# Optimization experiments

Measured on AMD Instinct MI355X. Metric: run time of the kernel, lower is better.

## Reference

```python
import jax, jax.numpy as jnp
import numpy as np

B, T, D = 16, 1024, 256
H, DK = 2, 128          # n_head, d_k = d_v = D // n_head
K = 5                   # conv kernel size
TEMP = float(np.sqrt(D))  # temperature = d_model ** 0.5


def mish(x):
    return x * jnp.tanh(jax.nn.softplus(x))


def setup_inputs() -> dict:
    key = jax.random.key(0)
    ks = jax.random.split(key, 16)
    s = 0.02
    p = lambda k, shp: jax.random.normal(k, shp, dtype=jnp.float32) * s
    inp = {
        'x': jax.random.normal(ks[0], (B, T, D), dtype=jnp.float32),
        'mask': jax.random.randint(ks[1], (B, T), 0, 2).astype(bool),
        # spectral MLP
        'W1': p(ks[2], (D, D)), 'b1': p(ks[3], (D,)),
        'W2': p(ks[4], (D, D)), 'b2': p(ks[5], (D,)),
        # two Conv1dGLU blocks: Conv1d(D -> 2D, k=5), torch layout [out,in,k]
        'cW1': p(ks[6], (2 * D, D, K)), 'cb1': p(ks[7], (2 * D,)),
        'cW2': p(ks[8], (2 * D, D, K)), 'cb2': p(ks[9], (2 * D,)),
        # attention projections (torch Linear: y = x @ W.T + b)
        'Wq': p(ks[10], (D, D)), 'bq': p(ks[11], (D,)),
        'Wk': p(ks[12], (D, D)), 'bk': p(ks[13], (D,)),
        'Wv': p(ks[14], (D, D)), 'bv': p(ks[15], (D,)),
        'Wo': p(jax.random.fold_in(key, 100), (D, D)),
        'bo': p(jax.random.fold_in(key, 101), (D,)),
        # final fc
        'Wf': p(jax.random.fold_in(key, 102), (D, D)),
        'bf': p(jax.random.fold_in(key, 103), (D,)),
    }
    return inp


def conv1d_glu(h, w, b):
    # h: [B, C, T]; w: [2C, C, K]; 'same' padding, GLU gate + residual
    y = jax.lax.conv_general_dilated(h, w, window_strides=(1,), padding=[(K // 2, K // 2)],
                                     dimension_numbers=('NCH', 'OIH', 'NCH'))
    y = y + b[None, :, None]
    a, g = jnp.split(y, 2, axis=1)
    return h + a * jax.nn.sigmoid(g)


def reference(x, mask, W1, b1, W2, b2, cW1, cb1, cW2, cb2,
              Wq, bq, Wk, bk, Wv, bv, Wo, bo, Wf, bf):
    # spectral: Linear + Mish (dropout is identity at inference)
    h = mish(x @ W1.T + b1)
    h = mish(h @ W2.T + b2)
    # temporal: two Conv1dGLU residual blocks over [B, C, T]
    h = h.transpose(0, 2, 1)
    h = conv1d_glu(h, cW1, cb1)
    h = conv1d_glu(h, cW2, cb2)
    h = h.transpose(0, 2, 1)
    # zero out padded frames
    h = jnp.where(mask[:, :, None], 0.0, h)
    residual = h
    # multi-head self-attention; mask hides padded keys
    q = (h @ Wq.T + bq).reshape(B, T, H, DK)
    k = (h @ Wk.T + bk).reshape(B, T, H, DK)
    v = (h @ Wv.T + bv).reshape(B, T, H, DK)
    attn = jnp.einsum('bqhd,bkhd->bhqk', q, k) / TEMP
    attn = jnp.where(mask[:, None, None, :], -jnp.inf, attn)
    attn = jax.nn.softmax(attn, axis=-1)
    out = jnp.einsum('bhqk,bkhd->bqhd', attn, v).reshape(B, T, D)
    h = out @ Wo.T + bo + residual
    # final projection + masked temporal average pool
    y = h @ Wf.T + bf
    len_ = (~mask).sum(axis=1, keepdims=True).astype(y.dtype)  # [B,1]
    y = jnp.where(mask[:, :, None], 0.0, y)
    w = y.sum(axis=1) / len_
    return w
```

## Files before the change

### kernel.cpp

```cpp
#include <hip/hip_runtime.h>
#include <hip/hip_bf16.h>
#include <math.h>


#define DEV __device__ __forceinline__

static constexpr int B_ = 16, T_ = 1024, D_ = 256;
static constexpr int N_ = B_ * T_;

typedef __attribute__((ext_vector_type(8))) short bf16x8;
typedef __attribute__((ext_vector_type(16))) float floatx16;

DEV float sigmoidf_(float x) { return 1.f / (1.f + __expf(-x)); }
DEV float mishf_(float x) {
  float u = __expf(fminf(x, 30.f));
  float t = u * (u + 2.f);
  return x * (t / (t + 2.f));
}
DEV ushort f2bf_(float x) {
  __hip_bfloat16 h = __float2bfloat16(x);
  return *(ushort*)&h;
}

__global__ __launch_bounds__(256) void prep_all_kernel(
    const unsigned* __restrict__ mraw,
    const float* __restrict__ W1, const float* __restrict__ W2,
    const float* __restrict__ Wq, const float* __restrict__ Wk,
    const float* __restrict__ Wv, const float* __restrict__ Wo,
    const float* __restrict__ cW1, const float* __restrict__ cW2,
    ushort* __restrict__ w1, ushort* __restrict__ w2,
    ushort* __restrict__ wqkv, ushort* __restrict__ wo,
    ushort* __restrict__ WtF1, ushort* __restrict__ WtF2,
    float* __restrict__ fmask, ushort* __restrict__ QF,
    ushort* __restrict__ KF, float* __restrict__ pooled) {
  int bid = blockIdx.x, tid = threadIdx.x;
  if (bid < 384) {
    int i = bid * 256 + tid;
    int widx = i >> 14, r = i & 16383;
    const float* src;
    ushort* dst;
    switch (widx) {
      case 0: src = W1; dst = w1; break;
      case 1: src = W2; dst = w2; break;
      case 2: src = Wq; dst = wqkv; break;
      case 3: src = Wk; dst = wqkv + 65536; break;
      case 4: src = Wv; dst = wqkv + 131072; break;
      default: src = Wo; dst = wo; break;
    }
    float4 v = ((const float4*)src)[r];
    ushort4 u;
    u.x = f2bf_(v.x); u.y = f2bf_(v.y); u.z = f2bf_(v.z); u.w = f2bf_(v.w);
    ((ushort4*)dst)[r] = u;
  } else if (bid < 1024) {
    int idx = (bid - 384) * 256 + tid;
    const float* cw = (idx < 81920) ? cW1 : cW2;
    ushort* dst = (idx < 81920) ? WtF1 : WtF2;
    int i8 = (idx < 81920) ? idx : idx - 81920;
    int i = i8 * 8;
    int half = (i >> 3) & 1, m31 = (i >> 4) & 31;
    int frag = i >> 9;
    int ks = frag & 1, c = (frag >> 1) & 7, tap = (frag >> 4) % 5,
        cot = frag / 80;
    int co = cot * 32 + m31;
    int cin0 = c * 32 + ks * 16 + half * 8;
    ushort u[8];
#pragma unroll
    for (int j = 0; j < 8; ++j)
      u[j] = f2bf_(cw[(size_t)(co * 256 + cin0 + j) * 5 + tap]);
    *(uint4*)&dst[i] = *(uint4*)u;
  } else {
    int isByte = 0, isFloat = 0;
    for (int i = 0; i < 16; ++i) {
      unsigned v = mraw[tid * 16 + i];
      if (v == 0x3F800000u) isFloat = 1;
      else if (v > 1u) isByte = 1;
    }
    __shared__ int sByte, sFloat;
    if (tid == 0) { sByte = 0; sFloat = 0; }
    __syncthreads();
    if (isByte) atomicOr(&sByte, 1);
    if (isFloat) atomicOr(&sFloat, 1);
    __syncthreads();
    int mode = sFloat ? 2 : (sByte ? 1 : 0);
    int mb = bid - 1024;
    int id = mb * 256 + tid;
    int bh = id >> 10, t = id & 1023, b = bh >> 1;
    int gidx = b * 1024 + t;
    unsigned mv;
    if (mode == 1) mv = ((const unsigned char*)mraw)[gidx];
    else           mv = mraw[gidx];
    float fm = (mv != 0u) ? 1.f : 0.f;
    if ((bh & 1) == 0) fmask[gidx] = fm;
    if (mb < 16) pooled[mb * 256 + tid] = 0.f;
    size_t qb = ((size_t)(bh * 32 + (t >> 5)) * 9 + 8) * 512 + (t & 31) * 16;
    QF[qb] = f2bf_(1.f);
#pragma unroll
    for (int j = 1; j < 16; ++j) QF[qb + j] = 0;
    size_t kb = ((size_t)(bh * 32 + (t >> 5)) * 9 + 8) * 512 + (t & 31) * 16;
    KF[kb] = (fm != 0.f) ? f2bf_(-60000.f) : (ushort)0;
#pragma unroll
    for (int j = 1; j < 16; ++j) KF[kb + j] = 0;
  }
}

template <int ACT, int RESID, int OMODE, int AF32>
__global__ __launch_bounds__(256, 4) void gemm_mfma_kernel(
    const void* __restrict__ Av, const ushort* __restrict__ W16,
    const float* __restrict__ bias, const float* __restrict__ resid,
    const float* __restrict__ fmask,
    float* __restrict__ outf, ushort* __restrict__ outb) {
  __shared__ __align__(16) ushort As[2][32 * 72];
  int tid = threadIdx.x;
  int w = tid >> 6, lane = tid & 63;
  int m31 = lane & 31, half = lane >> 5;
  int n0 = blockIdx.x * 32;
  int col = blockIdx.y * 128 + w * 32 + m31;
  const ushort* A16 = (const ushort*)Av;
  const float* A32 = (const float*)Av;
  int srow = tid >> 3, spart = tid & 7;

  floatx16 acc;
#pragma unroll
  for (int i = 0; i < 16; ++i) acc[i] = 0.f;

  auto stageA = [&](int buf, int k0) {
    if (AF32) {
      float4 v0 = *(const float4*)&A32[(size_t)(n0 + srow) * 256 + k0 + spart * 8];
      float4 v1 = *(const float4*)&A32[(size_t)(n0 + srow) * 256 + k0 + spart * 8 + 4];
      ushort u[8];
      u[0] = f2bf_(v0.x); u[1] = f2bf_(v0.y); u[2] = f2bf_(v0.z); u[3] = f2bf_(v0.w);
      u[4] = f2bf_(v1.x); u[5] = f2bf_(v1.y); u[6] = f2bf_(v1.z); u[7] = f2bf_(v1.w);
      *(uint4*)&As[buf][srow * 72 + spart * 8] = *(uint4*)u;
    } else {
      *(uint4*)&As[buf][srow * 72 + spart * 8] =
          *(const uint4*)&A16[(size_t)(n0 + srow) * 256 + k0 + spart * 8];
    }
  };
  stageA(0, 0);
  bf16x8 bn[4];
#pragma unroll
  for (int ks = 0; ks < 4; ++ks)
    bn[ks] = *(const bf16x8*)&W16[(size_t)col * 256 + ks * 16 + half * 8];

  for (int c = 0; c < 4; ++c) {
    __syncthreads();
    if (c < 3) stageA((c + 1) & 1, (c + 1) * 64);
    bf16x8 bc[4] = {bn[0], bn[1], bn[2], bn[3]};
    if (c < 3) {
      int k0 = (c + 1) * 64;
#pragma unroll
      for (int ks = 0; ks < 4; ++ks)
        bn[ks] = *(const bf16x8*)&W16[(size_t)col * 256 + k0 + ks * 16 + half * 8];
    }
    const ushort* ab = As[c & 1];
#pragma unroll
    for (int ks = 0; ks < 4; ++ks) {
      bf16x8 af = *(const bf16x8*)&ab[m31 * 72 + ks * 16 + half * 8];
      acc = __builtin_amdgcn_mfma_f32_32x32x16_bf16(af, bc[ks], acc, 0, 0, 0);
    }
  }
  float bv = bias[col];
  if (OMODE == 3) {
    int b = n0 >> 10;
    float psum = 0.f;
#pragma unroll
    for (int reg = 0; reg < 16; ++reg) {
      int row = n0 + (reg & 3) + 8 * (reg >> 2) + 4 * half;
      float keep = (fmask[row] == 0.f) ? 1.f : 0.f;
      psum += keep * (acc[reg] + bv + resid[(size_t)row * 256 + col]);
    }
    atomicAdd(&outf[b * 256 + col], psum);
    return;
  }
#pragma unroll
  for (int reg = 0; reg < 16; ++reg) {
    int row = n0 + (reg & 3) + 8 * (reg >> 2) + 4 * half;
    float v = acc[reg] + bv;
    if (ACT == 1) v = mishf_(v);
    if (RESID) v += resid[(size_t)row * 256 + col];
    if (OMODE == 0) {
      outf[(size_t)row * 256 + col] = v;
    } else if (OMODE == 1) {
      outb[(size_t)row * 256 + col] = f2bf_(v);
    } else {
      outf[(size_t)row * 256 + col] = v;
      outb[(size_t)row * 256 + col] = f2bf_(v);
    }
  }
}

__global__ __launch_bounds__(256, 4) void qkv_mfma_kernel(
    const ushort* __restrict__ A16, const ushort* __restrict__ wqkv,
    const float* __restrict__ bq, const float* __restrict__ bk,
    const float* __restrict__ bv,
    ushort* __restrict__ QF, ushort* __restrict__ KF, ushort* __restrict__ VF) {
  __shared__ __align__(16) ushort As[2][32 * 72];
  __shared__ __align__(16) ushort Tw[4][32 * 40];
  int tid = threadIdx.x;
  int w = tid >> 6, lane = tid & 63;
  int m31 = lane & 31, half = lane >> 5;
  int n0 = blockIdx.x * 32;
  int by = blockIdx.z;
  const ushort* W16 = wqkv + (size_t)by * 65536;
  const float* bias = (by == 0) ? bq : (by == 1) ? bk : bv;
  int col = blockIdx.y * 128 + w * 32 + m31;
  int srow = tid >> 3, spart = tid & 7;

  floatx16 acc;
#pragma unroll
  for (int i = 0; i < 16; ++i) acc[i] = 0.f;

  *(uint4*)&As[0][srow * 72 + spart * 8] =
      *(const uint4*)&A16[(size_t)(n0 + srow) * 256 + spart * 8];
  bf16x8 bn[4];
#pragma unroll
  for (int ks = 0; ks < 4; ++ks)
    bn[ks] = *(const bf16x8*)&W16[(size_t)col * 256 + ks * 16 + half * 8];

  for (int c = 0; c < 4; ++c) {
    __syncthreads();
    if (c < 3) {
      int k0 = (c + 1) * 64;
      *(uint4*)&As[(c + 1) & 1][srow * 72 + spart * 8] =
          *(const uint4*)&A16[(size_t)(n0 + srow) * 256 + k0 + spart * 8];
    }
    bf16x8 bc[4] = {bn[0], bn[1], bn[2], bn[3]};
    if (c < 3) {
      int k0 = (c + 1) * 64;
#pragma unroll
      for (int ks = 0; ks < 4; ++ks)
        bn[ks] = *(const bf16x8*)&W16[(size_t)col * 256 + k0 + ks * 16 + half * 8];
    }
    const ushort* ab = As[c & 1];
#pragma unroll
    for (int ks = 0; ks < 4; ++ks) {
      bf16x8 af = *(const bf16x8*)&ab[m31 * 72 + ks * 16 + half * 8];
      acc = __builtin_amdgcn_mfma_f32_32x32x16_bf16(af, bc[ks], acc, 0, 0, 0);
    }
  }
  int b = n0 >> 10;
  float bvv = bias[col];
  int h = col >> 7, d127 = col & 127;
  int bh = b * 2 + h;
  if (by == 2) {
    int ctv = d127 >> 5, m31v = d127 & 31;
#pragma unroll
    for (int rg = 0; rg < 4; ++rg) {
      int t0 = (n0 & 1023) + 8 * rg + 4 * half;
      ushort4 u;
      u.x = f2bf_(acc[rg * 4 + 0] + bvv);
      u.y = f2bf_(acc[rg * 4 + 1] + bvv);
      u.z = f2bf_(acc[rg * 4 + 2] + bvv);
      u.w = f2bf_(acc[rg * 4 + 3] + bvv);
      size_t addr = ((size_t)(bh * 16 + (t0 >> 6)) * 16 +
                     ((t0 >> 4) & 3) * 4 + ctv) * 512 +
                    m31v * 16 + ((t0 >> 3) & 1) * 8 + (t0 & 7);
      *(ushort4*)&VF[addr] = u;
    }
  } else {
    float scale = (by == 0) ? 0.0625f : 1.f;
    ushort* tw = &Tw[w][0];
#pragma unroll
    for (int reg = 0; reg < 16; ++reg) {
      int brow = (reg & 3) + 8 * (reg >> 2) + 4 * half;
      tw[brow * 40 + m31] = f2bf_((acc[reg] + bvv) * scale);
    }
    ushort* dst = (by == 0) ? QF : KF;
    int tile9 = (bh * 32 + ((n0 & 1023) >> 5)) * 9;
    int c0 = ((blockIdx.y * 128 + w * 32) & 127) >> 4;
    int tr = lane >> 1, hb = lane & 1;
#pragma unroll
    for (int cc = 0; cc < 2; ++cc) {
      uint4 v = *(const uint4*)&tw[tr * 40 + cc * 16 + hb * 8];
      *(uint4*)&dst[(size_t)(tile9 + c0 + cc) * 512 + lane * 8] = v;
    }
  }
}

template <int DO_MASK>
__global__ __launch_bounds__(256, 4) void conv_mfma_kernel(
    const ushort* __restrict__ H16, const float* __restrict__ Hf,
    const ushort* __restrict__ WtF, const float* __restrict__ cb,
    const float* __restrict__ fmask, float* __restrict__ outf,
    ushort* __restrict__ outb) {
  __shared__ __align__(16) ushort As[2][68 * 72];
  int tid = threadIdx.x;
  int w = tid >> 6, lane = tid & 63;
  int m31 = lane & 31, half = lane >> 5;
  int wr = w >> 1, wc = w & 1;
  int n0 = blockIdx.x * 64;
  int cg = blockIdx.y;
  int tbase = n0 & 1023;
  int acol = cg * 64 + wc * 32;
  int cotA = cg * 2 + wc, cotG = 8 + cg * 2 + wc;

  floatx16 acc[2];
#pragma unroll
  for (int ct = 0; ct < 2; ++ct)
#pragma unroll
    for (int i = 0; i < 16; ++i) acc[ct][i] = 0.f;

  auto stageA = [&](int buf, int k0) {
    for (int i = tid; i < 544; i += 256) {
      int row = i >> 3, part = i & 7;
      int t = tbase + row - 2;
      uint4 v = make_uint4(0u, 0u, 0u, 0u);
      if ((unsigned)t < 1024u)
        v = *(const uint4*)&H16[(size_t)(n0 + row - 2) * 256 + k0 + part * 8];
      *(uint4*)&As[buf][row * 72 + part * 8] = v;
    }
  };
  stageA(0, 0);

  for (int c = 0; c < 4; ++c) {
    __syncthreads();
    if (c < 3) stageA((c + 1) & 1, (c + 1) * 64);
    const ushort* ab = As[c & 1];
#pragma unroll
    for (int tap = 0; tap < 5; ++tap) {
      int fA = ((cotA * 5 + tap) * 8 + c * 2) * 2;
      int fG = ((cotG * 5 + tap) * 8 + c * 2) * 2;
      bf16x8 ba[4], bg[4];
#pragma unroll
      for (int q = 0; q < 4; ++q) {
        ba[q] = *(const bf16x8*)&WtF[(size_t)(fA + q) * 512 + m31 * 16 + half * 8];
        bg[q] = *(const bf16x8*)&WtF[(size_t)(fG + q) * 512 + m31 * 16 + half * 8];
      }
#pragma unroll
      for (int ks = 0; ks < 4; ++ks) {
        bf16x8 af = *(const bf16x8*)&ab[(wr * 32 + m31 + tap) * 72 +
                                        ks * 16 + half * 8];
        acc[0] = __builtin_amdgcn_mfma_f32_32x32x16_bf16(af, ba[ks], acc[0], 0, 0, 0);
        acc[1] = __builtin_amdgcn_mfma_f32_32x32x16_bf16(af, bg[ks], acc[1], 0, 0, 0);
      }
    }
  }
  int col = acol + m31;
  float ba = cb[col], bg = cb[256 + col];
#pragma unroll
  for (int reg = 0; reg < 16; ++reg) {
    int brow = wr * 32 + (reg & 3) + 8 * (reg >> 2) + 4 * half;
    int grow = n0 + brow;
    float a = acc[0][reg] + ba;
    float g = acc[1][reg] + bg;
    float v = Hf[(size_t)grow * 256 + col] + a * sigmoidf_(g);
    if (DO_MASK) {
      if (fmask[grow] != 0.f) v = 0.f;
    }
    outf[(size_t)grow * 256 + col] = v;
    outb[(size_t)grow * 256 + col] = f2bf_(v);
  }
}

__global__ __launch_bounds__(256, 2) void attn_mfma4_kernel(
    const ushort* __restrict__ QF, const ushort* __restrict__ KF,
    const ushort* __restrict__ VF, ushort* __restrict__ O) {
  __shared__ __align__(16) ushort Sm[2][17408];
  __shared__ float Ml[2][2][32];
  int tid = threadIdx.x;
  int w = tid >> 6, lane = tid & 63;
  int m31 = lane & 31, half = lane >> 5;
  int qt = w & 1, kh = w >> 1;
  int bh = blockIdx.x;
  int q0 = blockIdx.y * 64 + qt * 32;
  int lpos = m31 * 16 + half * 8;

  bf16x8 qe[9];
  {
    int qtile9 = (bh * 32 + (q0 >> 5)) * 9;
#pragma unroll
    for (int c = 0; c < 9; ++c)
      qe[c] = *(const bf16x8*)&QF[(size_t)(qtile9 + c) * 512 + lpos];
  }
  floatx16 oacc[4];
#pragma unroll
  for (int ct = 0; ct < 4; ++ct)
#pragma unroll
    for (int i = 0; i < 16; ++i) oacc[ct][i] = 0.f;
  float mi = -1e30f, li = 0.f;

  auto stage = [&](int it, int buf) {
    const ushort* k0src = KF + (size_t)(bh * 32 + it) * 4608;
    const ushort* k1src = KF + (size_t)(bh * 32 + 16 + it) * 4608;
    const ushort* v0src =
        VF + (size_t)((bh * 16 + (it >> 1)) * 16 + (it & 1) * 8) * 512;
    const ushort* v1src =
        VF + (size_t)((bh * 16 + 8 + (it >> 1)) * 16 + (it & 1) * 8) * 512;
    auto copyc = [&](int c) {
      const ushort* src;
      int idx;
      if (c < 576)       { src = k0src; idx = c; }
      else if (c < 1152) { src = k1src; idx = c - 576; }
      else if (c < 1664) { src = v0src; idx = c - 1152; }
      else               { src = v1src; idx = c - 1664; }
      uint4 v = *(const uint4*)(src + idx * 8);
      *(uint4*)&Sm[buf][c * 8] = v;
    };
#pragma unroll
    for (int k = 0; k < 8; ++k) copyc(tid + k * 256);
    if (tid < 128) copyc(2048 + tid);
  };

  stage(0, 0);
  for (int it = 0; it < 16; ++it) {
    __syncthreads();
    int buf = it & 1;
    const ushort* Kb = &Sm[buf][kh * 4608];
    const ushort* Vb = &Sm[buf][9216 + kh * 4096];
    floatx16 s0;
#pragma unroll
    for (int i = 0; i < 16; ++i) s0[i] = 0.f;
#pragma unroll
    for (int c = 0; c < 9; ++c) {
      bf16x8 kf = *(const bf16x8*)&Kb[c * 512 + lpos];
      s0 = __builtin_amdgcn_mfma_f32_32x32x16_bf16(kf, qe[c], s0, 0, 0, 0);
    }
    float mloc = s0[0];
#pragma unroll
    for (int r = 1; r < 16; ++r) mloc = fmaxf(mloc, s0[r]);
    float mt = fmaxf(mloc, __shfl_xor(mloc, 32));
    float mnew = fmaxf(mi, mt);
    float alpha = __expf(mi - mnew);
    bool dead = (mnew <= -3.0e4f);
    float sum = 0.f;
#pragma unroll
    for (int r = 0; r < 16; ++r) {
      float v = dead ? 0.f : __expf(s0[r] - mnew);
      s0[r] = v;
      sum += v;
    }
    sum += __shfl_xor(sum, 32);
    li = li * alpha + sum;
    mi = mnew;
#pragma unroll
    for (int ct = 0; ct < 4; ++ct)
#pragma unroll
      for (int i = 0; i < 16; ++i) oacc[ct][i] *= alpha;
    float tx[16];
#pragma unroll
    for (int r = 0; r < 16; ++r) tx[r] = __shfl_xor(s0[r], 32);
    bf16x8 pf[2];
#pragma unroll
    for (int s = 0; s < 2; ++s) {
      union { bf16x8 v; ushort u[8]; } pk;
#pragma unroll
      for (int j = 0; j < 8; ++j) {
        int base = s * 8;
        float own = s0[base + j];
        float lo = (j < 4) ? own : tx[base + j - 4];
        float hi = (j < 4) ? tx[base + 4 + j] : own;
        pk.u[j] = f2bf_(half ? hi : lo);
      }
      pf[s] = pk.v;
    }
#pragma unroll
    for (int s2 = 0; s2 < 2; ++s2)
#pragma unroll
      for (int ct = 0; ct < 4; ++ct) {
        bf16x8 vf = *(const bf16x8*)&Vb[(s2 * 4 + ct) * 512 + lpos];
        oacc[ct] = __builtin_amdgcn_mfma_f32_32x32x16_bf16(
            vf, pf[s2], oacc[ct], 0, 0, 0);
      }
    if (it < 15) stage(it + 1, (it + 1) & 1);
  }
  float* Opf = (float*)&Sm[0][0];
  if (kh == 1) {
#pragma unroll
    for (int ct = 0; ct < 4; ++ct)
#pragma unroll
      for (int r = 0; r < 16; ++r) {
        int dv = ct * 32 + (r & 3) + 8 * (r >> 2) + 4 * half;
        Opf[(qt * 128 + dv) * 33 + m31] = oacc[ct][r];
      }
    if (half == 0) { Ml[qt][0][m31] = mi; Ml[qt][1][m31] = li; }
  }
  __syncthreads();
  if (kh == 0) {
    float mB = Ml[qt][0][m31], lB = Ml[qt][1][m31];
    float m = fmaxf(mi, mB);
    float aA = __expf(mi - m), aB = __expf(mB - m);
    float l = li * aA + lB * aB;
    float inv = (l > 0.f) ? 1.f / l : 0.f;
    int b = bh >> 1, h = bh & 1;
    size_t rowbase = (size_t)(b * 1024 + q0 + m31) * 256 + h * 128;
#pragma unroll
    for (int ct = 0; ct < 4; ++ct)
#pragma unroll
      for (int rg = 0; rg < 4; ++rg) {
        int dv0 = ct * 32 + 8 * rg + 4 * half;
        ushort4 u;
        u.x = f2bf_((oacc[ct][rg * 4 + 0] * aA + Opf[(qt * 128 + dv0 + 0) * 33 + m31] * aB) * inv);
        u.y = f2bf_((oacc[ct][rg * 4 + 1] * aA + Opf[(qt * 128 + dv0 + 1) * 33 + m31] * aB) * inv);
        u.z = f2bf_((oacc[ct][rg * 4 + 2] * aA + Opf[(qt * 128 + dv0 + 2) * 33 + m31] * aB) * inv);
        u.w = f2bf_((oacc[ct][rg * 4 + 3] * aA + Opf[(qt * 128 + dv0 + 3) * 33 + m31] * aB) * inv);
        *(ushort4*)&O[rowbase + dv0] = u;
      }
  }
}

__global__ __launch_bounds__(256) void final_kernel(
    const float* __restrict__ pooled, const float* __restrict__ fmask,
    const float* __restrict__ Wf, const float* __restrict__ bf,
    float* __restrict__ out) {
  int b = blockIdx.x, j = threadIdx.x;
  __shared__ __align__(16) float p[256];
  __shared__ float red[256];
  p[j] = pooled[b * 256 + j];
  float c = 0.f;
  for (int i = 0; i < 4; ++i)
    c += (fmask[b * 1024 + i * 256 + j] == 0.f) ? 1.f : 0.f;
  red[j] = c;
  __syncthreads();
  for (int st = 128; st > 0; st >>= 1) {
    if (j < st) red[j] += red[j + st];
    __syncthreads();
  }
  float len = red[0];
  const float* wrow = Wf + (size_t)j * 256;
  float acc = 0.f;
  for (int d4 = 0; d4 < 64; ++d4) {
    float4 wv = ((const float4*)wrow)[d4];
    float4 pv = ((const float4*)p)[d4];
    acc += wv.x * pv.x + wv.y * pv.y + wv.z * pv.z + wv.w * pv.w;
  }
  float inv = (len > 0.f) ? 1.f / len : 0.f;
  out[b * 256 + j] = acc * inv + bf[j];
}

extern "C" void kernel_launch(void* const* d_in, const int* in_sizes, int n_in,
                              void* d_out, int out_size, void* d_ws, size_t ws_size,
                              hipStream_t stream) {
  const float* x      = (const float*)d_in[0];
  const unsigned* msk = (const unsigned*)d_in[1];
  const float* W1 = (const float*)d_in[2];
  const float* b1 = (const float*)d_in[3];
  const float* W2 = (const float*)d_in[4];
  const float* b2 = (const float*)d_in[5];
  const float* cW1 = (const float*)d_in[6];
  const float* cb1 = (const float*)d_in[7];
  const float* cW2 = (const float*)d_in[8];
  const float* cb2 = (const float*)d_in[9];
  const float* Wq = (const float*)d_in[10];
  const float* bq = (const float*)d_in[11];
  const float* Wk = (const float*)d_in[12];
  const float* bk = (const float*)d_in[13];
  const float* Wv = (const float*)d_in[14];
  const float* bv = (const float*)d_in[15];
  const float* Wo = (const float*)d_in[16];
  const float* bo = (const float*)d_in[17];
  const float* Wf = (const float*)d_in[18];
  const float* bf = (const float*)d_in[19];
  float* out = (float*)d_out;

  float* ws = (float*)d_ws;
  size_t ND = (size_t)N_ * D_;
  float* F0      = ws;
  float* F1      = F0 + ND;
  float* fmask   = F1 + ND;
  float* pooled  = fmask + N_;
  ushort* G0 = (ushort*)(pooled + 16 * 256);
  ushort* G1 = G0 + ND;
  ushort* QF = G1 + ND;
  ushort* KF = QF + (size_t)32 * 32 * 9 * 512;
  ushort* VF = KF + (size_t)32 * 32 * 9 * 512;
  ushort* w1_16 = VF + (size_t)32 * 16 * 16 * 512;
  ushort* w2_16 = w1_16 + 65536;
  ushort* wo_16 = w2_16 + 65536;
  ushort* wqkv  = wo_16 + 65536;
  ushort* WtF1  = wqkv + 3 * 65536;
  ushort* WtF2  = WtF1 + 655360;

  dim3 blk(256);
  prep_all_kernel<<<dim3(1152), blk, 0, stream>>>(
      msk, W1, W2, Wq, Wk, Wv, Wo, cW1, cW2,
      w1_16, w2_16, wqkv, wo_16, WtF1, WtF2, fmask, QF, KF, pooled);
  gemm_mfma_kernel<1, 0, 1, 1><<<dim3(512, 2), blk, 0, stream>>>(
      x, w1_16, b1, nullptr, nullptr, nullptr, G1);
  gemm_mfma_kernel<1, 0, 2, 0><<<dim3(512, 2), blk, 0, stream>>>(
      G1, w2_16, b2, nullptr, nullptr, F0, G0);
  conv_mfma_kernel<0><<<dim3(256, 4), blk, 0, stream>>>(
      G0, F0, WtF1, cb1, fmask, F1, G1);
  conv_mfma_kernel<1><<<dim3(256, 4), blk, 0, stream>>>(
      G1, F1, WtF2, cb2, fmask, F0, G0);
  qkv_mfma_kernel<<<dim3(512, 2, 3), blk, 0, stream>>>(
      G0, wqkv, bq, bk, bv, QF, KF, VF);
  attn_mfma4_kernel<<<dim3(32, 16), blk, 0, stream>>>(QF, KF, VF, G1);
  gemm_mfma_kernel<0, 1, 3, 0><<<dim3(512, 2), blk, 0, stream>>>(
      G1, wo_16, bo, F0, fmask, pooled, nullptr);
  final_kernel<<<dim3(16), blk, 0, stream>>>(pooled, fmask, Wf, bf, out);
}
```

Baseline: 282.6 us.

## Split global-to-LDS staging into register prefetch and deferred LDS write

In the GEMM, QKV projection, conv-GLU and attention kernels, the next tile's global loads are now issued into registers at the top of each iteration. They are written to shared memory only after the MFMA work on the current tile finishes. The aim is to hide global-load latency behind compute instead of stalling on each load before its LDS store. This raises register pressure, which can lower occupancy, notably the 9 uint4 staging registers in the attention kernel.

```diff
diff --git a/kernel.cpp b/kernel.cpp
--- a/kernel.cpp
+++ b/kernel.cpp
@@ -123,20 +123,28 @@
 #pragma unroll
   for (int i = 0; i < 16; ++i) acc[i] = 0.f;
 
-  auto stageA = [&](int buf, int k0) {
+  uint4 areg;
+  float4 af0, af1;
+  auto loadA = [&](int k0) {
     if (AF32) {
-      float4 v0 = *(const float4*)&A32[(size_t)(n0 + srow) * 256 + k0 + spart * 8];
-      float4 v1 = *(const float4*)&A32[(size_t)(n0 + srow) * 256 + k0 + spart * 8 + 4];
+      af0 = *(const float4*)&A32[(size_t)(n0 + srow) * 256 + k0 + spart * 8];
+      af1 = *(const float4*)&A32[(size_t)(n0 + srow) * 256 + k0 + spart * 8 + 4];
+    } else {
+      areg = *(const uint4*)&A16[(size_t)(n0 + srow) * 256 + k0 + spart * 8];
+    }
+  };
+  auto writeA = [&](int buf) {
+    if (AF32) {
       ushort u[8];
-      u[0] = f2bf_(v0.x); u[1] = f2bf_(v0.y); u[2] = f2bf_(v0.z); u[3] = f2bf_(v0.w);
-      u[4] = f2bf_(v1.x); u[5] = f2bf_(v1.y); u[6] = f2bf_(v1.z); u[7] = f2bf_(v1.w);
+      u[0] = f2bf_(af0.x); u[1] = f2bf_(af0.y); u[2] = f2bf_(af0.z); u[3] = f2bf_(af0.w);
+      u[4] = f2bf_(af1.x); u[5] = f2bf_(af1.y); u[6] = f2bf_(af1.z); u[7] = f2bf_(af1.w);
       *(uint4*)&As[buf][srow * 72 + spart * 8] = *(uint4*)u;
     } else {
-      *(uint4*)&As[buf][srow * 72 + spart * 8] =
-          *(const uint4*)&A16[(size_t)(n0 + srow) * 256 + k0 + spart * 8];
+      *(uint4*)&As[buf][srow * 72 + spart * 8] = areg;
     }
   };
-  stageA(0, 0);
+  loadA(0);
+  writeA(0);
   bf16x8 bn[4];
 #pragma unroll
   for (int ks = 0; ks < 4; ++ks)
@@ -144,7 +152,7 @@
 
   for (int c = 0; c < 4; ++c) {
     __syncthreads();
-    if (c < 3) stageA((c + 1) & 1, (c + 1) * 64);
+    if (c < 3) loadA((c + 1) * 64);
     bf16x8 bc[4] = {bn[0], bn[1], bn[2], bn[3]};
     if (c < 3) {
       int k0 = (c + 1) * 64;
@@ -158,6 +166,7 @@
       bf16x8 af = *(const bf16x8*)&ab[m31 * 72 + ks * 16 + half * 8];
       acc = __builtin_amdgcn_mfma_f32_32x32x16_bf16(af, bc[ks], acc, 0, 0, 0);
     }
+    if (c < 3) writeA((c + 1) & 1);
   }
   float bv = bias[col];
   if (OMODE == 3) {
@@ -210,8 +219,8 @@
 #pragma unroll
   for (int i = 0; i < 16; ++i) acc[i] = 0.f;
 
-  *(uint4*)&As[0][srow * 72 + spart * 8] =
-      *(const uint4*)&A16[(size_t)(n0 + srow) * 256 + spart * 8];
+  uint4 areg = *(const uint4*)&A16[(size_t)(n0 + srow) * 256 + spart * 8];
+  *(uint4*)&As[0][srow * 72 + spart * 8] = areg;
   bf16x8 bn[4];
 #pragma unroll
   for (int ks = 0; ks < 4; ++ks)
@@ -221,8 +230,7 @@
     __syncthreads();
     if (c < 3) {
       int k0 = (c + 1) * 64;
-      *(uint4*)&As[(c + 1) & 1][srow * 72 + spart * 8] =
-          *(const uint4*)&A16[(size_t)(n0 + srow) * 256 + k0 + spart * 8];
+      areg = *(const uint4*)&A16[(size_t)(n0 + srow) * 256 + k0 + spart * 8];
     }
     bf16x8 bc[4] = {bn[0], bn[1], bn[2], bn[3]};
     if (c < 3) {
@@ -237,6 +245,7 @@
       bf16x8 af = *(const bf16x8*)&ab[m31 * 72 + ks * 16 + half * 8];
       acc = __builtin_amdgcn_mfma_f32_32x32x16_bf16(af, bc[ks], acc, 0, 0, 0);
     }
+    if (c < 3) *(uint4*)&As[(c + 1) & 1][srow * 72 + spart * 8] = areg;
   }
   int b = n0 >> 10;
   float bvv = bias[col];
@@ -300,21 +309,37 @@
 #pragma unroll
     for (int i = 0; i < 16; ++i) acc[ct][i] = 0.f;
 
-  auto stageA = [&](int buf, int k0) {
-    for (int i = tid; i < 544; i += 256) {
-      int row = i >> 3, part = i & 7;
-      int t = tbase + row - 2;
-      uint4 v = make_uint4(0u, 0u, 0u, 0u);
-      if ((unsigned)t < 1024u)
-        v = *(const uint4*)&H16[(size_t)(n0 + row - 2) * 256 + k0 + part * 8];
-      *(uint4*)&As[buf][row * 72 + part * 8] = v;
+  uint4 ar[3];
+  auto loadA = [&](int k0) {
+#pragma unroll
+    for (int j = 0; j < 3; ++j) {
+      int i = tid + j * 256;
+      if (i < 544) {
+        int row = i >> 3, part = i & 7;
+        int t = tbase + row - 2;
+        uint4 v = make_uint4(0u, 0u, 0u, 0u);
+        if ((unsigned)t < 1024u)
+          v = *(const uint4*)&H16[(size_t)(n0 + row - 2) * 256 + k0 + part * 8];
+        ar[j] = v;
+      }
     }
   };
-  stageA(0, 0);
+  auto writeA = [&](int buf) {
+#pragma unroll
+    for (int j = 0; j < 3; ++j) {
+      int i = tid + j * 256;
+      if (i < 544) {
+        int row = i >> 3, part = i & 7;
+        *(uint4*)&As[buf][row * 72 + part * 8] = ar[j];
+      }
+    }
+  };
+  loadA(0);
+  writeA(0);
 
   for (int c = 0; c < 4; ++c) {
     __syncthreads();
-    if (c < 3) stageA((c + 1) & 1, (c + 1) * 64);
+    if (c < 3) loadA((c + 1) * 64);
     const ushort* ab = As[c & 1];
 #pragma unroll
     for (int tap = 0; tap < 5; ++tap) {
@@ -334,6 +359,7 @@
         acc[1] = __builtin_amdgcn_mfma_f32_32x32x16_bf16(af, bg[ks], acc[1], 0, 0, 0);
       }
     }
+    if (c < 3) writeA((c + 1) & 1);
   }
   int col = acol + m31;
   float ba = cb[col], bg = cb[256 + col];
@@ -379,31 +405,41 @@
     for (int i = 0; i < 16; ++i) oacc[ct][i] = 0.f;
   float mi = -1e30f, li = 0.f;
 
-  auto stage = [&](int it, int buf) {
+  uint4 sreg[9];
+  auto loadStage = [&](int it) {
     const ushort* k0src = KF + (size_t)(bh * 32 + it) * 4608;
     const ushort* k1src = KF + (size_t)(bh * 32 + 16 + it) * 4608;
     const ushort* v0src =
         VF + (size_t)((bh * 16 + (it >> 1)) * 16 + (it & 1) * 8) * 512;
     const ushort* v1src =
         VF + (size_t)((bh * 16 + 8 + (it >> 1)) * 16 + (it & 1) * 8) * 512;
-    auto copyc = [&](int c) {
+#pragma unroll
+    for (int k = 0; k < 8; ++k) {
+      int c = tid + k * 256;
       const ushort* src;
       int idx;
       if (c < 576)       { src = k0src; idx = c; }
       else if (c < 1152) { src = k1src; idx = c - 576; }
       else if (c < 1664) { src = v0src; idx = c - 1152; }
       else               { src = v1src; idx = c - 1664; }
-      uint4 v = *(const uint4*)(src + idx * 8);
-      *(uint4*)&Sm[buf][c * 8] = v;
-    };
-#pragma unroll
-    for (int k = 0; k < 8; ++k) copyc(tid + k * 256);
-    if (tid < 128) copyc(2048 + tid);
+      sreg[k] = *(const uint4*)(src + idx * 8);
+    }
+    if (tid < 128) sreg[8] = *(const uint4*)(v1src + (2048 + tid - 1664) * 8);
   };
-
-  stage(0, 0);
+  auto writeStage = [&](int buf) {
+#pragma unroll
+    for (int k = 0; k < 8; ++k) {
+      int c = tid + k * 256;
+      *(uint4*)&Sm[buf][c * 8] = sreg[k];
+    }
+    if (tid < 128) *(uint4*)&Sm[buf][(2048 + tid) * 8] = sreg[8];
+  };
+
+  loadStage(0);
+  writeStage(0);
   for (int it = 0; it < 16; ++it) {
     __syncthreads();
+    if (it < 15) loadStage(it + 1);
     int buf = it & 1;
     const ushort* Kb = &Sm[buf][kh * 4608];
     const ushort* Vb = &Sm[buf][9216 + kh * 4096];
@@ -461,7 +497,7 @@
         oacc[ct] = __builtin_amdgcn_mfma_f32_32x32x16_bf16(
             vf, pf[s2], oacc[ct], 0, 0, 0);
       }
-    if (it < 15) stage(it + 1, (it + 1) & 1);
+    if (it < 15) writeStage((it + 1) & 1);
   }
   float* Opf = (float*)&Sm[0][0];
   if (kh == 1) {
```

Measured after the change: 323.4 us. 1.14x slower.
